# Kernel tuning notes

Hardware: AMD Instinct MI355X
Metric: run time of the kernel (lower is better)

Reference implementation:

```python
import jax, jax.numpy as jnp
import numpy as np

K = 512      # fixed candidate budget per pyramid level (batched stand-in for mask.nonzero)
THR = 0.5    # candidate threshold from `p > 0.5`
CUBE = 4     # z-2 : z+2 -> 4-voxel cube per axis


def _conv3d(x, w, b, stride):
    y = jax.lax.conv_general_dilated(
        x, w, (stride, stride, stride), 'SAME',
        dimension_numbers=('NCDHW', 'OIDHW', 'NCDHW'))
    return y + b[None, :, None, None, None]


def _up2(x):
    return jnp.repeat(jnp.repeat(jnp.repeat(x, 2, axis=2), 2, axis=3), 2, axis=4)


def _extract(p):
    # p: [1, C, D, H, W] -> (cubes [K, C, 4, 4, 4], valid [K])
    p0 = p[0]
    C, D, H, W = p0.shape
    score = p0.max(axis=0)                       # [D, H, W] peak over channels
    vals, idx = jax.lax.top_k(score.reshape(-1), K)
    valid = (vals > THR).astype(p0.dtype)        # mask out sub-threshold slots
    z = idx // (H * W)
    rem = idx % (H * W)
    y = rem // W
    x = rem % W
    zs = jnp.clip(z - 2, 0, D - CUBE)
    ys = jnp.clip(y - 2, 0, H - CUBE)
    xs = jnp.clip(x - 2, 0, W - CUBE)

    def cube(zi, yi, xi):
        return jax.lax.dynamic_slice(p0, (0, zi, yi, xi), (C, CUBE, CUBE, CUBE))

    return jax.vmap(cube)(zs, ys, xs), valid


def _lhi(cubes):
    # local intensity descriptor: per-channel mean + std over the cube
    m = cubes.mean(axis=(2, 3, 4))
    s = jnp.sqrt(cubes.var(axis=(2, 3, 4)) + 1e-6)
    return jnp.concatenate([m, s], axis=-1)      # [K, 2C]


def _forward(x, c1w, c1b, c2w, c2b, c3w, c3b,
             l1w, l1b, l2w, l2b, l3w, l3b, w1, b1, w2, b2):
    # Encoder3D: 3 strided conv blocks
    f1 = jax.nn.relu(_conv3d(x, c1w, c1b, 2))    # [1,16,48,96,96]
    f2 = jax.nn.relu(_conv3d(f1, c2w, c2b, 2))   # [1,32,24,48,48]
    f3 = jax.nn.relu(_conv3d(f2, c3w, c3b, 2))   # [1,64,12,24,24]
    # FeaturePyramid3D: laterals + top-down adds
    p3 = _conv3d(f3, l3w, l3b, 1)
    p2 = _conv3d(f2, l2w, l2b, 1) + _up2(p3)
    p1 = _conv3d(f1, l1w, l1b, 1) + _up2(p2)
    outs = []
    for p in (p1, p2, p3):
        cubes, valid = _extract(p)
        lhi = _lhi(cubes)                        # [K, 64]
        h = jax.nn.relu(lhi @ w1 + b1)
        o = (h @ w2 + b2) * valid[:, None]       # zero out invalid candidate slots
        outs.append(o)
    return jnp.concatenate(outs, axis=0)         # [3K, 2]


def setup_inputs() -> dict:
    key = jax.random.key(0)
    ks = jax.random.split(key, 10)

    def w(k, shape, scale):
        return jax.random.normal(k, shape, jnp.float32) * scale

    return {
        'x':   jax.random.normal(ks[0], (1, 1, 96, 192, 192), jnp.float32),
        'c1w': w(ks[1], (16, 1, 3, 3, 3), 0.3),  'c1b': jnp.zeros((16,), jnp.float32),
        'c2w': w(ks[2], (32, 16, 3, 3, 3), 0.1), 'c2b': jnp.zeros((32,), jnp.float32),
        'c3w': w(ks[3], (64, 32, 3, 3, 3), 0.08), 'c3b': jnp.zeros((64,), jnp.float32),
        'l1w': w(ks[4], (32, 16, 1, 1, 1), 0.3), 'l1b': jnp.zeros((32,), jnp.float32),
        'l2w': w(ks[5], (32, 32, 1, 1, 1), 0.3), 'l2b': jnp.zeros((32,), jnp.float32),
        'l3w': w(ks[6], (32, 64, 1, 1, 1), 0.3), 'l3b': jnp.zeros((32,), jnp.float32),
        'w1':  w(ks[7], (64, 128), 0.2),         'b1':  jnp.zeros((128,), jnp.float32),
        'w2':  w(ks[8], (128, 2), 0.2),          'b2':  jnp.zeros((2,), jnp.float32),
    }


def reference(x, c1w, c1b, c2w, c2b, c3w, c3b,
              l1w, l1b, l2w, l2b, l3w, l3b, w1, b1, w2, b2):
    return _forward(x, c1w, c1b, c2w, c2b, c3w, c3b,
                    l1w, l1b, l2w, l2b, l3w, l3b, w1, b1, w2, b2)
```

## Files before the change

### kernel.cpp

```cpp
#include <hip/hip_runtime.h>
#include <hip/hip_bf16.h>
#include <cstdint>
#include <cstddef>

#define N1 442368
#define N2 55296
#define N3 6912

#define PZ1 9409
#define PN1 461041
#define PV1 461041
#define PZ2 2401
#define PN2 60025
#define PV2 60025

#define MAP1(x) (((x) & 1) ? 49 + ((x) >> 1) : ((x) >> 1))
#define MAP2(x) (((x) & 1) ? 25 + ((x) >> 1) : ((x) >> 1))

#define KCAND 512
#define CAP   4096

__device__ __forceinline__ unsigned long long f2key64(double f) {
  unsigned long long b = (unsigned long long)__double_as_longlong(f);
  return (b & 0x8000000000000000ULL) ? ~b : (b | 0x8000000000000000ULL);
}
__device__ __forceinline__ unsigned f2key32(float f) {
  unsigned b = __float_as_uint(f);
  return (b & 0x80000000u) ? ~b : (b | 0x80000000u);
}

__global__ void convert_k(const float* __restrict__ c1w, const float* __restrict__ c2w,
                          const float* __restrict__ c3w, const float* __restrict__ l1w,
                          const float* __restrict__ l2w, const float* __restrict__ l3w,
                          double* __restrict__ wd1, double* __restrict__ wd2,
                          double* __restrict__ wd3, double* __restrict__ wl1,
                          double* __restrict__ wl2, double* __restrict__ wl3) {
  int seg = blockIdx.y;
  int i = blockIdx.x * 256 + threadIdx.x;
  if (seg == 0) {
    if (i < 432) { int c = i & 15, t = i >> 4; wd1[i] = (double)c1w[c * 27 + t]; }
  } else if (seg == 1) {
    if (i < 13824) {
      int c = i & 7, t = (i >> 3) % 27, ci = (i / 216) & 15, g = i / 3456;
      wd2[i] = (double)c2w[((g * 8 + c) * 16 + ci) * 27 + t];
    }
  } else if (seg == 2) {
    if (i < 55296) {
      int c = i & 3, t = (i >> 2) % 27, ci = (i / 108) & 15, gi = i / 1728;
      int g = gi & 15, cig = gi >> 4;
      wd3[i] = (double)c3w[((g * 4 + c) * 32 + cig * 16 + ci) * 27 + t];
    }
  } else if (seg == 3) {
    if (i < 512) { int c = i & 31, ci = i >> 5; wl1[i] = (double)l1w[c * 16 + ci]; }
  } else if (seg == 4) {
    if (i < 1024) { int c = i & 31, ci = i >> 5; wl2[i] = (double)l2w[c * 32 + ci]; }
  } else {
    if (i < 2048) { int c = i & 31, ci = i >> 5; wl3[i] = (double)l3w[c * 64 + ci]; }
  }
}

__global__ __launch_bounds__(256) void conv1_k(const float* __restrict__ x, const double* __restrict__ wd1,
                                               const float* __restrict__ b, double* __restrict__ f1) {
  int v = blockIdx.x * 256 + threadIdx.x;
  if (v >= PV1) return;
  int z = v / PZ1; int r = v % PZ1; int y = r / 97; int xo = r % 97;
  int ov = z * PZ1 + y * 97 + MAP1(xo);
  if (z >= 48 || y >= 96 || xo >= 96) {
#pragma unroll
    for (int c = 0; c < 16; c++) f1[(size_t)c * PN1 + ov] = 0.0;
    return;
  }
  float val[27];
#pragma unroll
  for (int dz = 0; dz < 3; dz++)
#pragma unroll
    for (int dy = 0; dy < 3; dy++)
#pragma unroll
      for (int dx = 0; dx < 3; dx++) {
        int zi = 2 * z + dz, yi = 2 * y + dy, xi = 2 * xo + dx;
        bool ok = (zi < 96) & (yi < 192) & (xi < 192);
        int zc = min(zi, 95), yc = min(yi, 191), xc = min(xi, 191);
        float t = x[(zc * 192 + yc) * 192 + xc];
        val[(dz * 3 + dy) * 3 + dx] = ok ? t : 0.0f;
      }
  double acc[16];
#pragma unroll
  for (int c = 0; c < 16; c++) acc[c] = (double)b[c];
#pragma unroll
  for (int t = 0; t < 27; t++) {
    double vv = (double)val[t];
#pragma unroll
    for (int c = 0; c < 16; c++) acc[c] = fma(vv, wd1[t * 16 + c], acc[c]);
  }
#pragma unroll
  for (int c = 0; c < 16; c++) f1[(size_t)c * PN1 + ov] = fmax(acc[c], 0.0);
}

__global__ __launch_bounds__(256) void conv2_k(const double* __restrict__ f1, const double* __restrict__ wd2,
                                               const float* __restrict__ b, double* __restrict__ f2) {
  int g = blockIdx.y;
  int v = blockIdx.x * 256 + threadIdx.x;
  if (v >= PV2) return;
  int z = v / PZ2; int r = v % PZ2; int y = r / 49; int xo = r % 49;
  int ov = z * PZ2 + y * 49 + MAP2(xo);
  if (z >= 24 || y >= 48 || xo >= 48) {
#pragma unroll
    for (int c = 0; c < 8; c++) f2[(size_t)(g * 8 + c) * PN2 + ov] = 0.0;
    return;
  }
  double acc[8];
#pragma unroll
  for (int c = 0; c < 8; c++) acc[c] = (double)b[g * 8 + c];
  const double* wp = wd2 + (size_t)g * 3456;
  const double* base = f1 + (size_t)(2 * z) * PZ1 + (2 * y) * 97;
  for (int ci = 0; ci < 16; ci++) {
    const double* fp = base + (size_t)ci * PN1;
    double vals[27];
#pragma unroll
    for (int dz = 0; dz < 3; dz++)
#pragma unroll
      for (int dy = 0; dy < 3; dy++) {
        const double* row = fp + dz * PZ1 + dy * 97;
        int o = (dz * 3 + dy) * 3;
        vals[o + 0] = row[xo];
        vals[o + 1] = row[49 + xo];
        vals[o + 2] = row[xo + 1];
      }
#pragma unroll
    for (int t = 0; t < 27; t++) {
      double vv = vals[t];
      const double* w8 = wp + (ci * 27 + t) * 8;
#pragma unroll
      for (int c = 0; c < 8; c++) acc[c] = fma(vv, w8[c], acc[c]);
    }
  }
#pragma unroll
  for (int c = 0; c < 8; c++) f2[(size_t)(g * 8 + c) * PN2 + ov] = fmax(acc[c], 0.0);
}

__global__ __launch_bounds__(256) void conv3_k(const double* __restrict__ f2, const double* __restrict__ wd3,
                                               const float* __restrict__ b, double* __restrict__ f3a,
                                               double* __restrict__ f3b) {
  int gi = blockIdx.y;
  int g = gi & 15, cig = gi >> 4;
  int v = blockIdx.x * 256 + threadIdx.x;
  if (v >= N3) return;
  int z = v / 576; int r = v % 576; int y = r / 24; int xo = r % 24;
  double acc[4];
#pragma unroll
  for (int c = 0; c < 4; c++) acc[c] = cig == 0 ? (double)b[g * 4 + c] : 0.0;
  const double* wp = wd3 + (size_t)gi * 1728;
  const double* base = f2 + (size_t)(cig * 16) * PN2 + (size_t)(2 * z) * PZ2 + (2 * y) * 49;
  for (int ci = 0; ci < 16; ci++) {
    const double* fp = base + (size_t)ci * PN2;
    double vals[27];
#pragma unroll
    for (int dz = 0; dz < 3; dz++)
#pragma unroll
      for (int dy = 0; dy < 3; dy++) {
        const double* row = fp + dz * PZ2 + dy * 49;
        int o = (dz * 3 + dy) * 3;
        vals[o + 0] = row[xo];
        vals[o + 1] = row[25 + xo];
        vals[o + 2] = row[xo + 1];
      }
#pragma unroll
    for (int t = 0; t < 27; t++) {
      double vv = vals[t];
      const double* w4 = wp + (ci * 27 + t) * 4;
#pragma unroll
      for (int c = 0; c < 4; c++) acc[c] = fma(vv, w4[c], acc[c]);
    }
  }
  double* dst = cig == 0 ? f3a : f3b;
#pragma unroll
  for (int c = 0; c < 4; c++) dst[(size_t)(g * 4 + c) * N3 + v] = acc[c];
}

__global__ __launch_bounds__(256) void p3_k(const double* __restrict__ f3a, const double* __restrict__ f3b,
                                            const double* __restrict__ wl3,
                                            const float* __restrict__ b, double* __restrict__ p3d,
                                            float* __restrict__ p3f, double* __restrict__ s3) {
  int v = blockIdx.x * 256 + threadIdx.x;
  if (v >= N3) return;
  double acc[32];
#pragma unroll
  for (int c = 0; c < 32; c++) acc[c] = (double)b[c];
  for (int ci = 0; ci < 64; ci++) {
    double vv = fmax(f3a[(size_t)ci * N3 + v] + f3b[(size_t)ci * N3 + v], 0.0);
    const double* wp = wl3 + ci * 32;
#pragma unroll
    for (int c = 0; c < 32; c++) acc[c] = fma(vv, wp[c], acc[c]);
  }
  double m = -1e300;
#pragma unroll
  for (int c = 0; c < 32; c++) {
    p3d[(size_t)c * N3 + v] = acc[c];
    p3f[(size_t)c * N3 + v] = (float)acc[c];
    m = fmax(m, acc[c]);
  }
  s3[v] = m;
}

__global__ __launch_bounds__(256) void p2_k(const double* __restrict__ f2, const double* __restrict__ wl2,
                                            const float* __restrict__ b, const double* __restrict__ p3d,
                                            double* __restrict__ p2d, float* __restrict__ p2f, double* __restrict__ s2) {
  int v = blockIdx.x * 256 + threadIdx.x;
  if (v >= N2) return;
  int z = v / (48 * 48); int r = v % (48 * 48); int y = r / 48; int xo = r % 48;
  int pidx = z * PZ2 + y * 49 + MAP2(xo);
  int up = ((z >> 1) * 24 + (y >> 1)) * 24 + (xo >> 1);
  double acc[32];
#pragma unroll
  for (int c = 0; c < 32; c++) acc[c] = (double)b[c];
  for (int ci = 0; ci < 32; ci++) {
    double vv = f2[(size_t)ci * PN2 + pidx];
    const double* wp = wl2 + ci * 32;
#pragma unroll
    for (int c = 0; c < 32; c++) acc[c] = fma(vv, wp[c], acc[c]);
  }
  double m = -1e300;
#pragma unroll
  for (int c = 0; c < 32; c++) {
    double o = acc[c] + p3d[(size_t)c * N3 + up];
    p2d[(size_t)c * N2 + v] = o;
    p2f[(size_t)c * N2 + v] = (float)o;
    m = fmax(m, o);
  }
  s2[v] = m;
}

__global__ __launch_bounds__(256) void p1_k(const double* __restrict__ f1, const double* __restrict__ wl1,
                                            const float* __restrict__ b, const double* __restrict__ p2d,
                                            double* __restrict__ s1) {
  int v = blockIdx.x * 256 + threadIdx.x;
  if (v >= N1) return;
  int z = v / (96 * 96); int r = v % (96 * 96); int y = r / 96; int xo = r % 96;
  int pidx = z * PZ1 + y * 97 + MAP1(xo);
  int up = ((z >> 1) * 48 + (y >> 1)) * 48 + (xo >> 1);
  double acc[32];
#pragma unroll
  for (int c = 0; c < 32; c++) acc[c] = (double)b[c];
  for (int ci = 0; ci < 16; ci++) {
    double vv = f1[(size_t)ci * PN1 + pidx];
    const double* wp = wl1 + ci * 32;
#pragma unroll
    for (int c = 0; c < 32; c++) acc[c] = fma(vv, wp[c], acc[c]);
  }
  double m = -1e300;
#pragma unroll
  for (int c = 0; c < 32; c++) m = fmax(m, acc[c] + p2d[(size_t)c * N2 + up]);
  s1[v] = m;
}

__global__ void hist1_k(const double* __restrict__ s1, const double* __restrict__ s2,
                        const double* __restrict__ s3, unsigned* __restrict__ hist) {
  int L = blockIdx.y;
  const double* s = L == 0 ? s1 : (L == 1 ? s2 : s3);
  int n = L == 0 ? N1 : (L == 1 ? N2 : N3);
  unsigned* hg = hist + L * 256;
  __shared__ unsigned h[256];
  h[threadIdx.x] = 0;
  __syncthreads();
  for (int i = blockIdx.x * 256 + threadIdx.x; i < n; i += gridDim.x * 256)
    atomicAdd(&h[f2key32((float)s[i]) >> 24], 1u);
  __syncthreads();
  unsigned v = h[threadIdx.x];
  if (v) atomicAdd(&hg[threadIdx.x], v);
}

__global__ void hist2_k(const double* __restrict__ s1, const double* __restrict__ s2,
                        const double* __restrict__ s3, const unsigned* __restrict__ hist1,
                        unsigned* __restrict__ hist2) {
  int L = blockIdx.y;
  const double* s = L == 0 ? s1 : (L == 1 ? s2 : s3);
  int n = L == 0 ? N1 : (L == 1 ? N2 : N3);
  const unsigned* h1 = hist1 + L * 256;
  unsigned run = 0; unsigned b1 = 0;
  for (int i = 255; i >= 0; i--) {
    unsigned c = h1[i];
    if (run + c >= (unsigned)KCAND) { b1 = (unsigned)i; break; }
    run += c;
  }
  unsigned* hg = hist2 + L * 256;
  __shared__ unsigned h[256];
  h[threadIdx.x] = 0;
  __syncthreads();
  for (int i = blockIdx.x * 256 + threadIdx.x; i < n; i += gridDim.x * 256) {
    unsigned k = f2key32((float)s[i]);
    if ((k >> 24) == b1) atomicAdd(&h[(k >> 16) & 255u], 1u);
  }
  __syncthreads();
  unsigned v = h[threadIdx.x];
  if (v) atomicAdd(&hg[threadIdx.x], v);
}

__global__ void compact_k(const double* __restrict__ s1, const double* __restrict__ s2,
                          const double* __restrict__ s3, const unsigned* __restrict__ hist1,
                          const unsigned* __restrict__ hist2,
                          unsigned long long* __restrict__ ck, unsigned* __restrict__ cidx,
                          unsigned* __restrict__ cnt) {
  int L = blockIdx.y;
  const double* s = L == 0 ? s1 : (L == 1 ? s2 : s3);
  int n = L == 0 ? N1 : (L == 1 ? N2 : N3);
  const unsigned* h1 = hist1 + L * 256;
  const unsigned* h2 = hist2 + L * 256;
  unsigned run = 0; unsigned b1 = 0;
  for (int i = 255; i >= 0; i--) {
    unsigned c = h1[i];
    if (run + c >= (unsigned)KCAND) { b1 = (unsigned)i; break; }
    run += c;
  }
  unsigned b2 = 0;
  for (int i = 255; i >= 0; i--) {
    run += h2[i];
    if (run >= (unsigned)KCAND) { b2 = (unsigned)i; break; }
  }
  unsigned T = (b1 << 24) | (b2 << 16);
  for (int i = blockIdx.x * 256 + threadIdx.x; i < n; i += gridDim.x * 256) {
    double v = s[i];
    if (f2key32((float)v) >= T) {
      unsigned pos = atomicAdd(&cnt[L], 1u);
      if (pos < (unsigned)CAP) {
        ck[(size_t)L * CAP + pos] = f2key64(v);
        cidx[(size_t)L * CAP + pos] = (unsigned)i;
      }
    }
  }
}

__global__ void sort_k(const unsigned long long* __restrict__ ckA, const unsigned* __restrict__ cidxA,
                       const unsigned* __restrict__ cnt, uint2* __restrict__ topkA) {
  __shared__ unsigned long long k_[CAP];
  __shared__ unsigned x_[CAP];
  int L = blockIdx.x;
  const unsigned long long* ck = ckA + (size_t)L * CAP;
  const unsigned* cidx = cidxA + (size_t)L * CAP;
  uint2* topk = topkA + (size_t)L * KCAND;
  int t = threadIdx.x;
  unsigned m = cnt[L]; if (m > (unsigned)CAP) m = CAP;
  int sz = 512; while (sz < (int)m) sz <<= 1;
  for (int i = t; i < sz; i += 1024) {
    if (i < (int)m) { k_[i] = ck[i]; x_[i] = cidx[i]; }
    else            { k_[i] = 0ULL;  x_[i] = 0xFFFFFFFFu; }
  }
  __syncthreads();
  for (int kk = 2; kk <= sz; kk <<= 1) {
    for (int j = kk >> 1; j > 0; j >>= 1) {
      for (int i = t; i < sz; i += 1024) {
        int l = i ^ j;
        if (l > i) {
          unsigned long long ka = k_[i], kb = k_[l];
          unsigned ia = x_[i], ib = x_[l];
          bool b_first = (kb > ka) || (kb == ka && ib < ia);
          bool up = (i & kk) == 0;
          if (up == b_first) { k_[i] = kb; x_[i] = ib; k_[l] = ka; x_[l] = ia; }
        }
      }
      __syncthreads();
    }
  }
  if (t < KCAND) {
    unsigned long long key = k_[t];
    unsigned long long bb = (key >> 63) ? (key & 0x7FFFFFFFFFFFFFFFULL) : ~key;
    double sc = __longlong_as_double((long long)bb);
    topk[t] = make_uint2(x_[t], sc > 0.5 ? 1u : 0u);
  }
}

__global__ __launch_bounds__(64) void mlp_k(const uint2* __restrict__ topkA,
                                            const double* __restrict__ f1d, const double* __restrict__ p2d,
                                            const float* __restrict__ p2f, const float* __restrict__ p3f,
                                            const double* __restrict__ wl1, const float* __restrict__ l1b,
                                            const float* __restrict__ w1, const float* __restrict__ b1,
                                            const float* __restrict__ w2, const float* __restrict__ b2,
                                            float* __restrict__ out) {
  __shared__ double lhi[64];
  __shared__ double f1c[16 * 64];
  __shared__ double wsD[16 * 32];
  int L = blockIdx.y;
  int s = blockIdx.x;
  int D = 48 >> L, H = 96 >> L, W = 96 >> L;
  uint2 e = topkA[(size_t)L * KCAND + s];
  unsigned idx = e.x;
  double valid = e.y ? 1.0 : 0.0;
  int HW = H * W;
  int z = (int)(idx / (unsigned)HW);
  int r = (int)(idx % (unsigned)HW);
  int y = r / W; int x = r % W;
  int zs = min(max(z - 2, 0), D - 4);
  int ys = min(max(y - 2, 0), H - 4);
  int xs = min(max(x - 2, 0), W - 4);
  int t = threadIdx.x;
  int c = t & 31, h = t >> 5;
  double sum = 0.0, ss = 0.0;
  if (L == 0) {
    for (int i = t; i < 512; i += 64) wsD[i] = wl1[i];
    for (int i = t; i < 1024; i += 64) {
      int ci = i >> 6, v = i & 63;
      int dz = v >> 4, dy = (v >> 2) & 3, dx = v & 3;
      f1c[i] = f1d[(size_t)ci * PN1 + (zs + dz) * PZ1 + (ys + dy) * 97 + MAP1(xs + dx)];
    }
    __syncthreads();
    double bc = (double)l1b[c];
    for (int i = 0; i < 32; i++) {
      int vv = h * 32 + i;
      int dz = vv >> 4, dy = (vv >> 2) & 3, dx = vv & 3;
      int up = (((zs + dz) >> 1) * 48 + ((ys + dy) >> 1)) * 48 + ((xs + dx) >> 1);
      double val = bc + p2d[(size_t)c * N2 + up];
#pragma unroll
      for (int ci = 0; ci < 16; ci++)
        val = fma(f1c[ci * 64 + vv], wsD[ci * 32 + c], val);
      sum += val; ss = fma(val, val, ss);
    }
  } else {
    const float* p = (L == 1) ? p2f : p3f;
    const float* pc = p + (size_t)c * D * HW;
    for (int i = 0; i < 32; i++) {
      int vv = h * 32 + i;
      int dz = vv >> 4, dy = (vv >> 2) & 3, dx = vv & 3;
      double val = (double)pc[(zs + dz) * HW + (ys + dy) * W + (xs + dx)];
      sum += val; ss = fma(val, val, ss);
    }
  }
  sum += __shfl_xor(sum, 32);
  ss  += __shfl_xor(ss, 32);
  if (h == 0) {
    double mean = sum * (1.0 / 64.0);
    double var = ss * (1.0 / 64.0) - mean * mean;
    lhi[c] = mean;
    lhi[32 + c] = sqrt(var + 1e-6);
  }
  __syncthreads();
  double h0 = (double)b1[t], h1 = (double)b1[t + 64];
  for (int i = 0; i < 64; i++) {
    double li = lhi[i];
    h0 = fma(li, (double)w1[i * 128 + t], h0);
    h1 = fma(li, (double)w1[i * 128 + t + 64], h1);
  }
  h0 = fmax(h0, 0.0); h1 = fmax(h1, 0.0);
  double o0 = h0 * (double)w2[t * 2 + 0] + h1 * (double)w2[(t + 64) * 2 + 0];
  double o1 = h0 * (double)w2[t * 2 + 1] + h1 * (double)w2[(t + 64) * 2 + 1];
  for (int o = 1; o < 64; o <<= 1) { o0 += __shfl_xor(o0, o); o1 += __shfl_xor(o1, o); }
  if (t == 0) {
    out[((size_t)L * KCAND + s) * 2 + 0] = (float)((o0 + (double)b2[0]) * valid);
    out[((size_t)L * KCAND + s) * 2 + 1] = (float)((o1 + (double)b2[1]) * valid);
  }
}

extern "C" void kernel_launch(void* const* d_in, const int* in_sizes, int n_in,
                              void* d_out, int out_size, void* d_ws, size_t ws_size,
                              hipStream_t stream) {
  const float* x   = (const float*)d_in[0];
  const float* c1w = (const float*)d_in[1];  const float* c1b = (const float*)d_in[2];
  const float* c2w = (const float*)d_in[3];  const float* c2b = (const float*)d_in[4];
  const float* c3w = (const float*)d_in[5];  const float* c3b = (const float*)d_in[6];
  const float* l1w = (const float*)d_in[7];  const float* l1b = (const float*)d_in[8];
  const float* l2w = (const float*)d_in[9];  const float* l2b = (const float*)d_in[10];
  const float* l3w = (const float*)d_in[11]; const float* l3b = (const float*)d_in[12];
  const float* w1  = (const float*)d_in[13]; const float* b1  = (const float*)d_in[14];
  const float* w2  = (const float*)d_in[15]; const float* b2  = (const float*)d_in[16];
  float* out = (float*)d_out;

  char* ws = (char*)d_ws;
  size_t off = 0;
  auto take = [&](size_t bytes) { size_t o = off; off = (off + bytes + 255) & ~(size_t)255; return o; };
  double* f1d = (double*)(ws + take((size_t)16 * PN1 * 8));
  double* f2d = (double*)(ws + take((size_t)32 * PN2 * 8));
  double* f3a = (double*)(ws + take((size_t)64 * N3 * 8));
  double* f3b = (double*)(ws + take((size_t)64 * N3 * 8));
  double* p2d = (double*)(ws + take((size_t)32 * N2 * 8));
  float*  p2f = (float*) (ws + take((size_t)32 * N2 * 4));
  double* p3d = (double*)(ws + take((size_t)32 * N3 * 8));
  float*  p3f = (float*) (ws + take((size_t)32 * N3 * 4));
  double* s1 = (double*)(ws + take((size_t)N1 * 8));
  double* s2 = (double*)(ws + take((size_t)N2 * 8));
  double* s3 = (double*)(ws + take((size_t)N3 * 8));
  double* wd1 = (double*)(ws + take(432 * 8));
  double* wd2 = (double*)(ws + take(13824 * 8));
  double* wd3 = (double*)(ws + take(55296 * 8));
  double* wl1 = (double*)(ws + take(512 * 8));
  double* wl2 = (double*)(ws + take(1024 * 8));
  double* wl3 = (double*)(ws + take(2048 * 8));
  size_t zOff = take((3 * 256 + 3 * 256 + 3) * 4);
  unsigned* hist1 = (unsigned*)(ws + zOff);
  unsigned* hist2 = hist1 + 3 * 256;
  unsigned* cnt   = hist2 + 3 * 256;
  unsigned long long* candKey = (unsigned long long*)(ws + take((size_t)3 * CAP * 8));
  unsigned* candIdx = (unsigned*)(ws + take((size_t)3 * CAP * 4));
  uint2* topk = (uint2*)(ws + take((size_t)3 * KCAND * 8));

  hipMemsetAsync(ws + zOff, 0, (3 * 256 + 3 * 256 + 3) * 4, stream);

  convert_k<<<dim3(216, 6), 256, 0, stream>>>(c1w, c2w, c3w, l1w, l2w, l3w,
                                              wd1, wd2, wd3, wl1, wl2, wl3);
  conv1_k<<<(PV1 + 255) / 256, 256, 0, stream>>>(x, wd1, c1b, f1d);
  conv2_k<<<dim3((PV2 + 255) / 256, 4), 256, 0, stream>>>(f1d, wd2, c2b, f2d);
  conv3_k<<<dim3((N3 + 255) / 256, 32), 256, 0, stream>>>(f2d, wd3, c3b, f3a, f3b);
  p3_k<<<(N3 + 255) / 256, 256, 0, stream>>>(f3a, f3b, wl3, l3b, p3d, p3f, s3);
  p2_k<<<(N2 + 255) / 256, 256, 0, stream>>>(f2d, wl2, l2b, p3d, p2d, p2f, s2);
  p1_k<<<(N1 + 255) / 256, 256, 0, stream>>>(f1d, wl1, l1b, p2d, s1);

  hist1_k<<<dim3(64, 3), 256, 0, stream>>>(s1, s2, s3, hist1);
  hist2_k<<<dim3(64, 3), 256, 0, stream>>>(s1, s2, s3, hist1, hist2);
  compact_k<<<dim3(112, 3), 256, 0, stream>>>(s1, s2, s3, hist1, hist2, candKey, candIdx, cnt);
  sort_k<<<3, 1024, 0, stream>>>(candKey, candIdx, cnt, topk);
  mlp_k<<<dim3(KCAND, 3), 64, 0, stream>>>(topk, f1d, p2d, p2f, p3f, wl1, l1b,
                                           w1, b1, w2, b2, out);
}
```

Baseline: 374.1 us.

## Compute all conv2 output channels per thread, drop conv3 input-channel split, add float score copies

conv2 now computes all 32 output channels in one thread instead of splitting them into 4 groups of 8. Each input window is loaded once rather than four times, at the cost of 32 double accumulators and higher register pressure, with launch bounds raised to allow 2 blocks. conv3 drops its two-way input-channel split and partial-sum buffers and applies ReLU directly, which removes a buffer and the add in p3 but halves the number of blocks. The pyramid kernels also write float copies of the score maps, so the histogram and compaction passes read 4-byte values instead of doubles.

```diff
diff --git a/kernel.cpp b/kernel.cpp
--- a/kernel.cpp
+++ b/kernel.cpp
@@ -41,14 +41,13 @@
     if (i < 432) { int c = i & 15, t = i >> 4; wd1[i] = (double)c1w[c * 27 + t]; }
   } else if (seg == 1) {
     if (i < 13824) {
-      int c = i & 7, t = (i >> 3) % 27, ci = (i / 216) & 15, g = i / 3456;
-      wd2[i] = (double)c2w[((g * 8 + c) * 16 + ci) * 27 + t];
+      int c = i & 31, t = (i >> 5) % 27, ci = i / 864;
+      wd2[i] = (double)c2w[(c * 16 + ci) * 27 + t];
     }
   } else if (seg == 2) {
     if (i < 55296) {
-      int c = i & 3, t = (i >> 2) % 27, ci = (i / 108) & 15, gi = i / 1728;
-      int g = gi & 15, cig = gi >> 4;
-      wd3[i] = (double)c3w[((g * 4 + c) * 32 + cig * 16 + ci) * 27 + t];
+      int c = i & 3, t = (i >> 2) % 27, ci = (i / 108) & 31, g = i / 3456;
+      wd3[i] = (double)c3w[((g * 4 + c) * 32 + ci) * 27 + t];
     }
   } else if (seg == 3) {
     if (i < 512) { int c = i & 31, ci = i >> 5; wl1[i] = (double)l1w[c * 16 + ci]; }
@@ -96,22 +95,20 @@
   for (int c = 0; c < 16; c++) f1[(size_t)c * PN1 + ov] = fmax(acc[c], 0.0);
 }
 
-__global__ __launch_bounds__(256) void conv2_k(const double* __restrict__ f1, const double* __restrict__ wd2,
-                                               const float* __restrict__ b, double* __restrict__ f2) {
-  int g = blockIdx.y;
+__global__ __launch_bounds__(256, 2) void conv2_k(const double* __restrict__ f1, const double* __restrict__ wd2,
+                                                  const float* __restrict__ b, double* __restrict__ f2) {
   int v = blockIdx.x * 256 + threadIdx.x;
   if (v >= PV2) return;
   int z = v / PZ2; int r = v % PZ2; int y = r / 49; int xo = r % 49;
   int ov = z * PZ2 + y * 49 + MAP2(xo);
   if (z >= 24 || y >= 48 || xo >= 48) {
 #pragma unroll
-    for (int c = 0; c < 8; c++) f2[(size_t)(g * 8 + c) * PN2 + ov] = 0.0;
+    for (int c = 0; c < 32; c++) f2[(size_t)c * PN2 + ov] = 0.0;
     return;
   }
-  double acc[8];
-#pragma unroll
-  for (int c = 0; c < 8; c++) acc[c] = (double)b[g * 8 + c];
-  const double* wp = wd2 + (size_t)g * 3456;
+  double acc[32];
+#pragma unroll
+  for (int c = 0; c < 32; c++) acc[c] = (double)b[c];
   const double* base = f1 + (size_t)(2 * z) * PZ1 + (2 * y) * 97;
   for (int ci = 0; ci < 16; ci++) {
     const double* fp = base + (size_t)ci * PN1;
@@ -129,29 +126,27 @@
 #pragma unroll
     for (int t = 0; t < 27; t++) {
       double vv = vals[t];
-      const double* w8 = wp + (ci * 27 + t) * 8;
-#pragma unroll
-      for (int c = 0; c < 8; c++) acc[c] = fma(vv, w8[c], acc[c]);
-    }
-  }
-#pragma unroll
-  for (int c = 0; c < 8; c++) f2[(size_t)(g * 8 + c) * PN2 + ov] = fmax(acc[c], 0.0);
-}
-
-__global__ __launch_bounds__(256) void conv3_k(const double* __restrict__ f2, const double* __restrict__ wd3,
-                                               const float* __restrict__ b, double* __restrict__ f3a,
-                                               double* __restrict__ f3b) {
-  int gi = blockIdx.y;
-  int g = gi & 15, cig = gi >> 4;
+      const double* w32 = wd2 + (ci * 27 + t) * 32;
+#pragma unroll
+      for (int c = 0; c < 32; c++) acc[c] = fma(vv, w32[c], acc[c]);
+    }
+  }
+#pragma unroll
+  for (int c = 0; c < 32; c++) f2[(size_t)c * PN2 + ov] = fmax(acc[c], 0.0);
+}
+
+__global__ __launch_bounds__(256, 2) void conv3_k(const double* __restrict__ f2, const double* __restrict__ wd3,
+                                                  const float* __restrict__ b, double* __restrict__ f3) {
+  int g = blockIdx.y;
   int v = blockIdx.x * 256 + threadIdx.x;
   if (v >= N3) return;
   int z = v / 576; int r = v % 576; int y = r / 24; int xo = r % 24;
   double acc[4];
 #pragma unroll
-  for (int c = 0; c < 4; c++) acc[c] = cig == 0 ? (double)b[g * 4 + c] : 0.0;
-  const double* wp = wd3 + (size_t)gi * 1728;
-  const double* base = f2 + (size_t)(cig * 16) * PN2 + (size_t)(2 * z) * PZ2 + (2 * y) * 49;
-  for (int ci = 0; ci < 16; ci++) {
+  for (int c = 0; c < 4; c++) acc[c] = (double)b[g * 4 + c];
+  const double* wp = wd3 + (size_t)g * 3456;
+  const double* base = f2 + (size_t)(2 * z) * PZ2 + (2 * y) * 49;
+  for (int ci = 0; ci < 32; ci++) {
     const double* fp = base + (size_t)ci * PN2;
     double vals[27];
 #pragma unroll
@@ -172,22 +167,21 @@
       for (int c = 0; c < 4; c++) acc[c] = fma(vv, w4[c], acc[c]);
     }
   }
-  double* dst = cig == 0 ? f3a : f3b;
-#pragma unroll
-  for (int c = 0; c < 4; c++) dst[(size_t)(g * 4 + c) * N3 + v] = acc[c];
-}
-
-__global__ __launch_bounds__(256) void p3_k(const double* __restrict__ f3a, const double* __restrict__ f3b,
-                                            const double* __restrict__ wl3,
+#pragma unroll
+  for (int c = 0; c < 4; c++) f3[(size_t)(g * 4 + c) * N3 + v] = fmax(acc[c], 0.0);
+}
+
+__global__ __launch_bounds__(256) void p3_k(const double* __restrict__ f3, const double* __restrict__ wl3,
                                             const float* __restrict__ b, double* __restrict__ p3d,
-                                            float* __restrict__ p3f, double* __restrict__ s3) {
+                                            float* __restrict__ p3f, double* __restrict__ s3,
+                                            float* __restrict__ s3f) {
   int v = blockIdx.x * 256 + threadIdx.x;
   if (v >= N3) return;
   double acc[32];
 #pragma unroll
   for (int c = 0; c < 32; c++) acc[c] = (double)b[c];
   for (int ci = 0; ci < 64; ci++) {
-    double vv = fmax(f3a[(size_t)ci * N3 + v] + f3b[(size_t)ci * N3 + v], 0.0);
+    double vv = f3[(size_t)ci * N3 + v];
     const double* wp = wl3 + ci * 32;
 #pragma unroll
     for (int c = 0; c < 32; c++) acc[c] = fma(vv, wp[c], acc[c]);
@@ -200,11 +194,13 @@
     m = fmax(m, acc[c]);
   }
   s3[v] = m;
+  s3f[v] = (float)m;
 }
 
 __global__ __launch_bounds__(256) void p2_k(const double* __restrict__ f2, const double* __restrict__ wl2,
                                             const float* __restrict__ b, const double* __restrict__ p3d,
-                                            double* __restrict__ p2d, float* __restrict__ p2f, double* __restrict__ s2) {
+                                            double* __restrict__ p2d, float* __restrict__ p2f,
+                                            double* __restrict__ s2, float* __restrict__ s2f) {
   int v = blockIdx.x * 256 + threadIdx.x;
   if (v >= N2) return;
   int z = v / (48 * 48); int r = v % (48 * 48); int y = r / 48; int xo = r % 48;
@@ -228,11 +224,12 @@
     m = fmax(m, o);
   }
   s2[v] = m;
+  s2f[v] = (float)m;
 }
 
 __global__ __launch_bounds__(256) void p1_k(const double* __restrict__ f1, const double* __restrict__ wl1,
                                             const float* __restrict__ b, const double* __restrict__ p2d,
-                                            double* __restrict__ s1) {
+                                            double* __restrict__ s1, float* __restrict__ s1f) {
   int v = blockIdx.x * 256 + threadIdx.x;
   if (v >= N1) return;
   int z = v / (96 * 96); int r = v % (96 * 96); int y = r / 96; int xo = r % 96;
@@ -251,29 +248,30 @@
 #pragma unroll
   for (int c = 0; c < 32; c++) m = fmax(m, acc[c] + p2d[(size_t)c * N2 + up]);
   s1[v] = m;
-}
-
-__global__ void hist1_k(const double* __restrict__ s1, const double* __restrict__ s2,
-                        const double* __restrict__ s3, unsigned* __restrict__ hist) {
+  s1f[v] = (float)m;
+}
+
+__global__ void hist1_k(const float* __restrict__ s1, const float* __restrict__ s2,
+                        const float* __restrict__ s3, unsigned* __restrict__ hist) {
   int L = blockIdx.y;
-  const double* s = L == 0 ? s1 : (L == 1 ? s2 : s3);
+  const float* s = L == 0 ? s1 : (L == 1 ? s2 : s3);
   int n = L == 0 ? N1 : (L == 1 ? N2 : N3);
   unsigned* hg = hist + L * 256;
   __shared__ unsigned h[256];
   h[threadIdx.x] = 0;
   __syncthreads();
   for (int i = blockIdx.x * 256 + threadIdx.x; i < n; i += gridDim.x * 256)
-    atomicAdd(&h[f2key32((float)s[i]) >> 24], 1u);
+    atomicAdd(&h[f2key32(s[i]) >> 24], 1u);
   __syncthreads();
   unsigned v = h[threadIdx.x];
   if (v) atomicAdd(&hg[threadIdx.x], v);
 }
 
-__global__ void hist2_k(const double* __restrict__ s1, const double* __restrict__ s2,
-                        const double* __restrict__ s3, const unsigned* __restrict__ hist1,
+__global__ void hist2_k(const float* __restrict__ s1, const float* __restrict__ s2,
+                        const float* __restrict__ s3, const unsigned* __restrict__ hist1,
                         unsigned* __restrict__ hist2) {
   int L = blockIdx.y;
-  const double* s = L == 0 ? s1 : (L == 1 ? s2 : s3);
+  const float* s = L == 0 ? s1 : (L == 1 ? s2 : s3);
   int n = L == 0 ? N1 : (L == 1 ? N2 : N3);
   const unsigned* h1 = hist1 + L * 256;
   unsigned run = 0; unsigned b1 = 0;
@@ -287,7 +285,7 @@
   h[threadIdx.x] = 0;
   __syncthreads();
   for (int i = blockIdx.x * 256 + threadIdx.x; i < n; i += gridDim.x * 256) {
-    unsigned k = f2key32((float)s[i]);
+    unsigned k = f2key32(s[i]);
     if ((k >> 24) == b1) atomicAdd(&h[(k >> 16) & 255u], 1u);
   }
   __syncthreads();
@@ -295,13 +293,16 @@
   if (v) atomicAdd(&hg[threadIdx.x], v);
 }
 
-__global__ void compact_k(const double* __restrict__ s1, const double* __restrict__ s2,
-                          const double* __restrict__ s3, const unsigned* __restrict__ hist1,
-                          const unsigned* __restrict__ hist2,
+__global__ void compact_k(const float* __restrict__ s1f, const float* __restrict__ s2f,
+                          const float* __restrict__ s3f,
+                          const double* __restrict__ s1d, const double* __restrict__ s2d,
+                          const double* __restrict__ s3d,
+                          const unsigned* __restrict__ hist1, const unsigned* __restrict__ hist2,
                           unsigned long long* __restrict__ ck, unsigned* __restrict__ cidx,
                           unsigned* __restrict__ cnt) {
   int L = blockIdx.y;
-  const double* s = L == 0 ? s1 : (L == 1 ? s2 : s3);
+  const float* s = L == 0 ? s1f : (L == 1 ? s2f : s3f);
+  const double* sd = L == 0 ? s1d : (L == 1 ? s2d : s3d);
   int n = L == 0 ? N1 : (L == 1 ? N2 : N3);
   const unsigned* h1 = hist1 + L * 256;
   const unsigned* h2 = hist2 + L * 256;
@@ -318,11 +319,10 @@
   }
   unsigned T = (b1 << 24) | (b2 << 16);
   for (int i = blockIdx.x * 256 + threadIdx.x; i < n; i += gridDim.x * 256) {
-    double v = s[i];
-    if (f2key32((float)v) >= T) {
+    if (f2key32(s[i]) >= T) {
       unsigned pos = atomicAdd(&cnt[L], 1u);
       if (pos < (unsigned)CAP) {
-        ck[(size_t)L * CAP + pos] = f2key64(v);
+        ck[(size_t)L * CAP + pos] = f2key64(sd[i]);
         cidx[(size_t)L * CAP + pos] = (unsigned)i;
       }
     }
@@ -467,8 +467,7 @@
   auto take = [&](size_t bytes) { size_t o = off; off = (off + bytes + 255) & ~(size_t)255; return o; };
   double* f1d = (double*)(ws + take((size_t)16 * PN1 * 8));
   double* f2d = (double*)(ws + take((size_t)32 * PN2 * 8));
-  double* f3a = (double*)(ws + take((size_t)64 * N3 * 8));
-  double* f3b = (double*)(ws + take((size_t)64 * N3 * 8));
+  double* f3d = (double*)(ws + take((size_t)64 * N3 * 8));
   double* p2d = (double*)(ws + take((size_t)32 * N2 * 8));
   float*  p2f = (float*) (ws + take((size_t)32 * N2 * 4));
   double* p3d = (double*)(ws + take((size_t)32 * N3 * 8));
@@ -476,6 +475,9 @@
   double* s1 = (double*)(ws + take((size_t)N1 * 8));
   double* s2 = (double*)(ws + take((size_t)N2 * 8));
   double* s3 = (double*)(ws + take((size_t)N3 * 8));
+  float* s1f = (float*)(ws + take((size_t)N1 * 4));
+  float* s2f = (float*)(ws + take((size_t)N2 * 4));
+  float* s3f = (float*)(ws + take((size_t)N3 * 4));
   double* wd1 = (double*)(ws + take(432 * 8));
   double* wd2 = (double*)(ws + take(13824 * 8));
   double* wd3 = (double*)(ws + take(55296 * 8));
@@ -495,15 +497,16 @@
   convert_k<<<dim3(216, 6), 256, 0, stream>>>(c1w, c2w, c3w, l1w, l2w, l3w,
                                               wd1, wd2, wd3, wl1, wl2, wl3);
   conv1_k<<<(PV1 + 255) / 256, 256, 0, stream>>>(x, wd1, c1b, f1d);
-  conv2_k<<<dim3((PV2 + 255) / 256, 4), 256, 0, stream>>>(f1d, wd2, c2b, f2d);
-  conv3_k<<<dim3((N3 + 255) / 256, 32), 256, 0, stream>>>(f2d, wd3, c3b, f3a, f3b);
-  p3_k<<<(N3 + 255) / 256, 256, 0, stream>>>(f3a, f3b, wl3, l3b, p3d, p3f, s3);
-  p2_k<<<(N2 + 255) / 256, 256, 0, stream>>>(f2d, wl2, l2b, p3d, p2d, p2f, s2);
-  p1_k<<<(N1 + 255) / 256, 256, 0, stream>>>(f1d, wl1, l1b, p2d, s1);
-
-  hist1_k<<<dim3(64, 3), 256, 0, stream>>>(s1, s2, s3, hist1);
-  hist2_k<<<dim3(64, 3), 256, 0, stream>>>(s1, s2, s3, hist1, hist2);
-  compact_k<<<dim3(112, 3), 256, 0, stream>>>(s1, s2, s3, hist1, hist2, candKey, candIdx, cnt);
+  conv2_k<<<(PV2 + 255) / 256, 256, 0, stream>>>(f1d, wd2, c2b, f2d);
+  conv3_k<<<dim3((N3 + 255) / 256, 16), 256, 0, stream>>>(f2d, wd3, c3b, f3d);
+  p3_k<<<(N3 + 255) / 256, 256, 0, stream>>>(f3d, wl3, l3b, p3d, p3f, s3, s3f);
+  p2_k<<<(N2 + 255) / 256, 256, 0, stream>>>(f2d, wl2, l2b, p3d, p2d, p2f, s2, s2f);
+  p1_k<<<(N1 + 255) / 256, 256, 0, stream>>>(f1d, wl1, l1b, p2d, s1, s1f);
+
+  hist1_k<<<dim3(64, 3), 256, 0, stream>>>(s1f, s2f, s3f, hist1);
+  hist2_k<<<dim3(64, 3), 256, 0, stream>>>(s1f, s2f, s3f, hist1, hist2);
+  compact_k<<<dim3(112, 3), 256, 0, stream>>>(s1f, s2f, s3f, s1, s2, s3, hist1, hist2,
+                                              candKey, candIdx, cnt);
   sort_k<<<3, 1024, 0, stream>>>(candKey, candIdx, cnt, topk);
   mlp_k<<<dim3(KCAND, 3), 64, 0, stream>>>(topk, f1d, p2d, p2f, p3f, wl1, l1b,
                                            w1, b1, w2, b2, out);
```

Measured after the change: 429.6 us. 1.15x slower.
